# Optimization experiments

Measured on AMD Instinct MI355X. Metric: run time of the kernel, lower is better.

## Reference

```python
import jax, jax.numpy as jnp
import numpy as np

NEG_SLOPE = 0.01  # torch leaky_relu default

def _lrelu(x):
    return jax.nn.leaky_relu(x, NEG_SLOPE)

def _l2norm(x, axis):
    # torch F.normalize(p=2, eps=1e-12)
    n = jnp.linalg.norm(x, axis=axis, keepdims=True)
    return x / jnp.maximum(n, 1e-12)

def setup_inputs() -> dict:
    key = jax.random.key(0)
    ks = jax.random.split(key, 12)
    Nda, Nq, C, Din, Dout = 10000, 64, 1024, 128, 256
    target_adj = (jax.random.uniform(ks[0], (Nda, Nda)) < 0.002).astype(jnp.float32)
    query_adj = (jax.random.uniform(ks[1], (Nq, Nq)) < 0.2).astype(jnp.float32)
    node_features_da = jax.random.normal(ks[2], (Nda, Din), dtype=jnp.float32)
    node_features_q = jax.random.normal(ks[3], (Nq, Din), dtype=jnp.float32)
    candidate_set = jax.random.randint(ks[4], (C,), 0, Nda)
    candidate_adj = (jax.random.uniform(ks[5], (C, C)) < 0.01).astype(jnp.float32)
    s_in = 1.0 / np.sqrt(Din).astype(np.float32)
    s_out = 1.0 / np.sqrt(Dout).astype(np.float32)
    W1_da = jax.random.normal(ks[6], (Din, Dout), dtype=jnp.float32) * s_in
    W1_q = jax.random.normal(ks[7], (Din, Dout), dtype=jnp.float32) * s_in
    W2_da = jax.random.normal(ks[8], (Dout, Dout), dtype=jnp.float32) * s_out
    W2_q = jax.random.normal(ks[9], (Dout, Dout), dtype=jnp.float32) * s_out
    threshold = jnp.float32(0.2)
    return {"target_adj": target_adj, "node_features_da": node_features_da,
            "query_adj": query_adj, "node_features_q": node_features_q,
            "candidate_set": candidate_set, "candidate_adj": candidate_adj,
            "threshold": threshold, "W1_da": W1_da, "W1_q": W1_q,
            "W2_da": W2_da, "W2_q": W2_q}

def _cross_cosine(q, da, candidate_set):
    # cosine similarity between each query node and each candidate target node: [Nq, C]
    return _l2norm(q, 1) @ _l2norm(da[candidate_set], 1).T

def reference(target_adj, node_features_da, query_adj, node_features_q,
              candidate_set, candidate_adj, threshold, W1_da, W1_q, W2_da, W2_q):
    # layer 1: GCN propagation on both graphs (gcn(adj,x) = adj @ x @ W)
    da1 = _lrelu(target_adj @ (node_features_da @ W1_da))   # [Nda, D]
    q1 = _lrelu(query_adj @ (node_features_q @ W1_q))       # [Nq, D]
    c1 = _cross_cosine(q1, da1, candidate_set)               # [Nq, C]
    pre_da1 = da1[candidate_set]                             # [C, D]
    # NOTE: da1[candidate_set].data = ... mutates a temporary in torch -> no-op on da1
    att_da1 = _lrelu(da1)                                    # dropout in eval = identity
    h1_q = c1 @ pre_da1                                      # [Nq, D]
    att_q1 = _lrelu(q1 + _l2norm(h1_q, 0))
    # layer 2
    da2 = _lrelu(target_adj @ (att_da1 @ W2_da))
    q2 = _lrelu(query_adj @ (att_q1 @ W2_q))
    c2 = _cross_cosine(q2, da2, candidate_set)
    pre_da2 = da2[candidate_set]
    att_da2 = _lrelu(da2)                                    # in-place update is again a no-op
    h2_q = c2 @ pre_da2
    att_q2 = _lrelu(q2 + _l2norm(h2_q, 0))
    # graph-level matching score per target node
    emb = jnp.mean(att_q2, axis=0, keepdims=True)            # [1, D]
    num = att_da2 @ emb[0]                                   # [Nda]
    den = jnp.maximum(jnp.linalg.norm(att_da2, axis=1) * jnp.linalg.norm(emb), 1e-8)
    end = (num / den)[None, :]                               # [1, Nda]
    # threshold selection expressed with a mask (jit-safe, same math: excluded
    # rows/cols are zero and do not affect L2 norms, sums, or the trace)
    m = (end[0] > threshold).astype(att_da2.dtype)           # [Nda]
    F_ = att_da2 * m[:, None]
    re_adj = F_ @ F_.T                                       # [Nda, Nda]
    nor_re = _l2norm(re_adj, 1) * target_adj                 # elementwise with original adj
    cnt = jnp.sum(m)
    total = jnp.sum(nor_re)
    tr = jnp.trace(nor_re)
    has = cnt > 0
    pre_avg_degree = jnp.where(has, total / jnp.maximum(cnt, 1.0), 0.0)
    pre_avg_nodes = jnp.where(has, tr, 0.0)
    pre_density = jnp.where(has, 2.0 * total / (tr * (tr - 1.0) + 1e-4), 0.0)
    return (end, att_da2, att_q2, pre_avg_degree, pre_density, pre_avg_nodes)
```

## Files before the change

### kernel.cpp

```cpp
#include <hip/hip_runtime.h>

constexpr int NDA = 10000;
constexpr int NQ  = 64;
constexpr int CND = 1024;
constexpr int DIN = 128;
constexpr int D   = 256;
constexpr int CAP = 96;

#define LRELU(x) ((x) >= 0.f ? (x) : 0.01f * (x))

__device__ __forceinline__ float wave_red64(float v) {
#pragma unroll
    for (int o = 32; o; o >>= 1) v += __shfl_down(v, o);
    return v;
}

__global__ __launch_bounds__(256) void build_csr(const float* __restrict__ adj,
                                                 int* __restrict__ cols,
                                                 int* __restrict__ rowcnt) {
    int row = blockIdx.x;
    __shared__ int scnt;
    if (threadIdx.x == 0) scnt = 0;
    __syncthreads();
    const float4* rp = (const float4*)(adj + (size_t)row * NDA);
    for (int i = threadIdx.x; i < NDA / 4; i += 256) {
        float4 v = rp[i];
        if (v.x != 0.f) { int s = atomicAdd(&scnt, 1); if (s < CAP) cols[row * CAP + s] = 4 * i; }
        if (v.y != 0.f) { int s = atomicAdd(&scnt, 1); if (s < CAP) cols[row * CAP + s] = 4 * i + 1; }
        if (v.z != 0.f) { int s = atomicAdd(&scnt, 1); if (s < CAP) cols[row * CAP + s] = 4 * i + 2; }
        if (v.w != 0.f) { int s = atomicAdd(&scnt, 1); if (s < CAP) cols[row * CAP + s] = 4 * i + 3; }
    }
    __syncthreads();
    if (threadIdx.x == 0) rowcnt[row] = min(scnt, CAP);
}

template <int W, bool RELU_IN>
__global__ void spmm(const int* __restrict__ cols,
                     const int* __restrict__ rowcnt,
                     const float* __restrict__ X,
                     float* __restrict__ out) {
    int row = blockIdx.x;
    int d = threadIdx.x;
    int cnt = rowcnt[row];
    __shared__ int sc[CAP];
    if (d < CAP && d < cnt) sc[d] = cols[row * CAP + d];
    __syncthreads();
    float a0 = 0.f, a1 = 0.f, a2 = 0.f, a3 = 0.f;
    int k = 0;
    for (; k + 4 <= cnt; k += 4) {
        float v0 = X[(size_t)sc[k + 0] * W + d];
        float v1 = X[(size_t)sc[k + 1] * W + d];
        float v2 = X[(size_t)sc[k + 2] * W + d];
        float v3 = X[(size_t)sc[k + 3] * W + d];
        if (RELU_IN) { v0 = LRELU(v0); v1 = LRELU(v1); v2 = LRELU(v2); v3 = LRELU(v3); }
        a0 += v0; a1 += v1; a2 += v2; a3 += v3;
    }
    for (; k < cnt; k++) {
        float v = X[(size_t)sc[k] * W + d];
        if (RELU_IN) v = LRELU(v);
        a0 += v;
    }
    out[(size_t)row * W + d] = (a0 + a1) + (a2 + a3);
}

template <bool RELU_C, bool DUAL>
__global__ __launch_bounds__(256) void gemm64(const float* __restrict__ A,
                                              const float* __restrict__ B,
                                              float* __restrict__ C,
                                              float* __restrict__ C2,
                                              int M, int N, int K) {
    __shared__ float As[16][68];
    __shared__ float Bs[16][68];
    const int bm = blockIdx.x * 64;
    const int bn = blockIdx.y * 64;
    const int tid = threadIdx.x;
    const int tx = tid & 15, ty = tid >> 4;
    float acc[4][4] = {};
    for (int k0 = 0; k0 < K; k0 += 16) {
        {
            int m = tid >> 2;
            int k4 = (tid & 3) * 4;
            float4 v = make_float4(0.f, 0.f, 0.f, 0.f);
            if (bm + m < M) v = *(const float4*)(A + (size_t)(bm + m) * K + k0 + k4);
            As[k4 + 0][m] = v.x; As[k4 + 1][m] = v.y; As[k4 + 2][m] = v.z; As[k4 + 3][m] = v.w;
        }
        {
            int kk = tid >> 4;
            int n4 = (tid & 15) * 4;
            float4 v = *(const float4*)(B + (size_t)(k0 + kk) * N + bn + n4);
            Bs[kk][n4 + 0] = v.x; Bs[kk][n4 + 1] = v.y; Bs[kk][n4 + 2] = v.z; Bs[kk][n4 + 3] = v.w;
        }
        __syncthreads();
#pragma unroll
        for (int kk = 0; kk < 16; kk++) {
            float av[4], bv[4];
#pragma unroll
            for (int i = 0; i < 4; i++) av[i] = As[kk][ty * 4 + i];
#pragma unroll
            for (int j = 0; j < 4; j++) bv[j] = Bs[kk][tx * 4 + j];
#pragma unroll
            for (int i = 0; i < 4; i++)
#pragma unroll
                for (int j = 0; j < 4; j++) acc[i][j] += av[i] * bv[j];
        }
        __syncthreads();
    }
#pragma unroll
    for (int i = 0; i < 4; i++) {
        int r = bm + ty * 4 + i;
        if (r < M) {
            float4 v;
            v.x = acc[i][0]; v.y = acc[i][1]; v.z = acc[i][2]; v.w = acc[i][3];
            if (RELU_C) { v.x = LRELU(v.x); v.y = LRELU(v.y); v.z = LRELU(v.z); v.w = LRELU(v.w); }
            *(float4*)(C + (size_t)r * N + bn + tx * 4) = v;
            if (DUAL) {
                float4 u;
                u.x = LRELU(v.x); u.y = LRELU(v.y); u.z = LRELU(v.z); u.w = LRELU(v.w);
                *(float4*)(C2 + (size_t)r * N + bn + tx * 4) = u;
            }
        }
    }
}

__global__ __launch_bounds__(256) void qpath_kernel(const float* __restrict__ Fq,
                                                    const float* __restrict__ Wq,
                                                    const float* __restrict__ Qadj,
                                                    float* __restrict__ q_out,
                                                    int K) {
    __shared__ float As[16][68];
    __shared__ float Bs[16][68];
    __shared__ float Xs[64][68];
    __shared__ float Qs[64][68];
    const int bn = blockIdx.x * 64;
    const int tid = threadIdx.x;
    const int tx = tid & 15, ty = tid >> 4;
    float acc[4][4] = {};
    for (int k0 = 0; k0 < K; k0 += 16) {
        {
            int m = tid >> 2;
            int k4 = (tid & 3) * 4;
            float4 v = *(const float4*)(Fq + (size_t)m * K + k0 + k4);
            As[k4 + 0][m] = v.x; As[k4 + 1][m] = v.y; As[k4 + 2][m] = v.z; As[k4 + 3][m] = v.w;
        }
        {
            int kk = tid >> 4;
            int n4 = (tid & 15) * 4;
            float4 v = *(const float4*)(Wq + (size_t)(k0 + kk) * D + bn + n4);
            Bs[kk][n4 + 0] = v.x; Bs[kk][n4 + 1] = v.y; Bs[kk][n4 + 2] = v.z; Bs[kk][n4 + 3] = v.w;
        }
        __syncthreads();
#pragma unroll
        for (int kk = 0; kk < 16; kk++) {
            float av[4], bv[4];
#pragma unroll
            for (int i = 0; i < 4; i++) av[i] = As[kk][ty * 4 + i];
#pragma unroll
            for (int j = 0; j < 4; j++) bv[j] = Bs[kk][tx * 4 + j];
#pragma unroll
            for (int i = 0; i < 4; i++)
#pragma unroll
                for (int j = 0; j < 4; j++) acc[i][j] += av[i] * bv[j];
        }
        __syncthreads();
    }
#pragma unroll
    for (int i = 0; i < 4; i++)
#pragma unroll
        for (int j = 0; j < 4; j++) Xs[ty * 4 + i][tx * 4 + j] = acc[i][j];
    for (int l = tid; l < NQ * NQ; l += 256) Qs[l >> 6][l & 63] = Qadj[l];
    __syncthreads();
    float a2[4][4] = {};
#pragma unroll 4
    for (int kk = 0; kk < NQ; kk++) {
        float av[4], bv[4];
#pragma unroll
        for (int i = 0; i < 4; i++) av[i] = Qs[ty * 4 + i][kk];
#pragma unroll
        for (int j = 0; j < 4; j++) bv[j] = Xs[kk][tx * 4 + j];
#pragma unroll
        for (int i = 0; i < 4; i++)
#pragma unroll
            for (int j = 0; j < 4; j++) a2[i][j] += av[i] * bv[j];
    }
#pragma unroll
    for (int i = 0; i < 4; i++)
#pragma unroll
        for (int j = 0; j < 4; j++)
            q_out[(ty * 4 + i) * D + bn + tx * 4 + j] = LRELU(a2[i][j]);
}

__global__ __launch_bounds__(256) void rownorms_kernel(const float* __restrict__ da,
                                                       const int* __restrict__ cand,
                                                       float* __restrict__ rncinv,
                                                       const float* __restrict__ q,
                                                       float* __restrict__ rnqinv) {
    int b = blockIdx.x;
    const float* src;
    float* dst;
    if (b < CND) { src = da + (size_t)cand[b] * D; dst = rncinv + b; }
    else         { src = q + (size_t)(b - CND) * D; dst = rnqinv + (b - CND); }
    float v = src[threadIdx.x];
    float p = wave_red64(v * v);
    __shared__ float red[4];
    int w = threadIdx.x >> 6, lane = threadIdx.x & 63;
    if (lane == 0) red[w] = p;
    __syncthreads();
    if (threadIdx.x == 0) *dst = 1.f / fmaxf(sqrtf(red[0] + red[1] + red[2] + red[3]), 1e-12f);
}

__global__ __launch_bounds__(256) void candM_kernel(const float* __restrict__ da,
                                                    const int* __restrict__ cand,
                                                    const float* __restrict__ rncinv,
                                                    float* __restrict__ M) {
    __shared__ float SA[8][64], SB[8][64];
    const int ti = blockIdx.x, tj = blockIdx.y;
    const int tid = threadIdx.x;
    const int tx = tid & 15, ty = tid >> 4;
    float acc[4][4] = {};
    for (int c0 = 0; c0 < CND; c0 += 8) {
        for (int l = tid; l < 512; l += 256) {
            int rr = l >> 6, c = l & 63;
            int cr = cand[c0 + rr];
            float s = rncinv[c0 + rr];
            SA[rr][c] = da[(size_t)cr * D + ti * 64 + c] * s;
            SB[rr][c] = da[(size_t)cr * D + tj * 64 + c];
        }
        __syncthreads();
#pragma unroll
        for (int rr = 0; rr < 8; rr++) {
            float av[4], bv[4];
#pragma unroll
            for (int i = 0; i < 4; i++) av[i] = SA[rr][ty * 4 + i];
#pragma unroll
            for (int j = 0; j < 4; j++) bv[j] = SB[rr][tx * 4 + j];
#pragma unroll
            for (int i = 0; i < 4; i++)
#pragma unroll
                for (int j = 0; j < 4; j++) acc[i][j] += av[i] * bv[j];
        }
        __syncthreads();
    }
#pragma unroll
    for (int i = 0; i < 4; i++)
#pragma unroll
        for (int j = 0; j < 4; j++)
            M[(ti * 64 + ty * 4 + i) * D + tj * 64 + tx * 4 + j] = acc[i][j];
}

__global__ __launch_bounds__(256) void hq_gemm(const float* __restrict__ q,
                                               const float* __restrict__ rnqinv,
                                               const float* __restrict__ M,
                                               float* __restrict__ h) {
    __shared__ float As[16][68];
    __shared__ float Bs[16][68];
    const int bn = blockIdx.x * 64;
    const int tid = threadIdx.x;
    const int tx = tid & 15, ty = tid >> 4;
    float acc[4][4] = {};
    for (int k0 = 0; k0 < D; k0 += 16) {
        {
            int m = tid >> 2;
            int k4 = (tid & 3) * 4;
            float s = rnqinv[m];
            float4 v = *(const float4*)(q + (size_t)m * D + k0 + k4);
            As[k4 + 0][m] = v.x * s; As[k4 + 1][m] = v.y * s;
            As[k4 + 2][m] = v.z * s; As[k4 + 3][m] = v.w * s;
        }
        {
            int kk = tid >> 4;
            int n4 = (tid & 15) * 4;
            float4 v = *(const float4*)(M + (size_t)(k0 + kk) * D + bn + n4);
            Bs[kk][n4 + 0] = v.x; Bs[kk][n4 + 1] = v.y; Bs[kk][n4 + 2] = v.z; Bs[kk][n4 + 3] = v.w;
        }
        __syncthreads();
#pragma unroll
        for (int kk = 0; kk < 16; kk++) {
            float av[4], bv[4];
#pragma unroll
            for (int i = 0; i < 4; i++) av[i] = As[kk][ty * 4 + i];
#pragma unroll
            for (int j = 0; j < 4; j++) bv[j] = Bs[kk][tx * 4 + j];
#pragma unroll
            for (int i = 0; i < 4; i++)
#pragma unroll
                for (int j = 0; j < 4; j++) acc[i][j] += av[i] * bv[j];
        }
        __syncthreads();
    }
#pragma unroll
    for (int i = 0; i < 4; i++)
#pragma unroll
        for (int j = 0; j < 4; j++)
            h[(ty * 4 + i) * D + bn + tx * 4 + j] = acc[i][j];
}

__global__ __launch_bounds__(256) void attq_kernel(const float* __restrict__ q,
                                                   const float* __restrict__ h,
                                                   float* __restrict__ attq,
                                                   float* __restrict__ emb) {
    int d = threadIdx.x;
    float hv[NQ];
    float ss = 0.f;
#pragma unroll
    for (int r = 0; r < NQ; r++) {
        hv[r] = h[r * D + d];
        ss += hv[r] * hv[r];
    }
    float inv = 1.f / fmaxf(sqrtf(ss), 1e-12f);
    float es = 0.f;
#pragma unroll
    for (int r = 0; r < NQ; r++) {
        float v = q[r * D + d] + hv[r] * inv;
        v = LRELU(v);
        attq[r * D + d] = v;
        es += v;
    }
    if (emb) {
        float e = es * (1.f / (float)NQ);
        emb[d] = e;
        float p = wave_red64(e * e);
        __shared__ float red[4];
        int w = d >> 6, lane = d & 63;
        if (lane == 0) red[w] = p;
        __syncthreads();
        if (d == 0) emb[D] = sqrtf(red[0] + red[1] + red[2] + red[3]);
    }
}

__global__ __launch_bounds__(256) void end_kernel(const float* __restrict__ A,
                                                  const float* __restrict__ emb,
                                                  const float* __restrict__ thr_p,
                                                  float* __restrict__ endv,
                                                  float* __restrict__ m,
                                                  float* __restrict__ cnt) {
    __shared__ float se[D];
    __shared__ float scnt;
    int d = threadIdx.x;
    se[d] = emb[d];
    if (d == 0) scnt = 0.f;
    __syncthreads();
    float embn = emb[D];
    float thr = *thr_p;
    int w = d >> 6, lane = d & 63;
    int row = blockIdx.x * 4 + w;
    const float* ar = A + (size_t)row * D;
    float num = 0.f, sq = 0.f;
#pragma unroll
    for (int s = 0; s < 4; s++) {
        float v = ar[lane + 64 * s];
        num += v * se[lane + 64 * s];
        sq += v * v;
    }
#pragma unroll
    for (int o = 32; o; o >>= 1) { num += __shfl_down(num, o); sq += __shfl_down(sq, o); }
    if (lane == 0) {
        float den = fmaxf(sqrtf(sq) * embn, 1e-8f);
        float e = num / den;
        endv[row] = e;
        float mv = e > thr ? 1.f : 0.f;
        m[row] = mv;
        if (mv != 0.f) atomicAdd(&scnt, 1.f);
    }
    __syncthreads();
    if (d == 0 && scnt != 0.f) atomicAdd(cnt, scnt);
}

constexpr int GCHUNK = 400;
__global__ __launch_bounds__(256) void G_kernel(const float* __restrict__ A,
                                                const float* __restrict__ m,
                                                float* __restrict__ G) {
    __shared__ float SA[8][64], SB[8][64];
    int ti = blockIdx.x >> 2, tj = blockIdx.x & 3;
    int base = blockIdx.y * GCHUNK;
    int tid = threadIdx.x;
    int tx = tid & 15, ty = tid >> 4;
    float acc[4][4] = {};
    for (int g0 = 0; g0 < GCHUNK; g0 += 8) {
        for (int l = tid; l < 512; l += 256) {
            int rr = l >> 6, c = l & 63;
            int r = base + g0 + rr;
            float mv = m[r];
            SA[rr][c] = A[(size_t)r * D + ti * 64 + c] * mv;
            SB[rr][c] = A[(size_t)r * D + tj * 64 + c];
        }
        __syncthreads();
#pragma unroll
        for (int rr = 0; rr < 8; rr++) {
            float av[4], bv[4];
#pragma unroll
            for (int i = 0; i < 4; i++) av[i] = SA[rr][ty * 4 + i];
#pragma unroll
            for (int j = 0; j < 4; j++) bv[j] = SB[rr][tx * 4 + j];
#pragma unroll
            for (int i = 0; i < 4; i++)
#pragma unroll
                for (int j = 0; j < 4; j++) acc[i][j] += av[i] * bv[j];
        }
        __syncthreads();
    }
#pragma unroll
    for (int i = 0; i < 4; i++)
#pragma unroll
        for (int j = 0; j < 4; j++)
            atomicAdd(&G[(ti * 64 + ty * 4 + i) * D + tj * 64 + tx * 4 + j], acc[i][j]);
}

__global__ __launch_bounds__(256) void final_kernel(const int* __restrict__ cols,
                                                    const int* __restrict__ rowcnt,
                                                    const float* __restrict__ m,
                                                    const float* __restrict__ A,
                                                    const float* __restrict__ H,
                                                    double* __restrict__ total,
                                                    double* __restrict__ tr) {
    int i = blockIdx.x;
    if (m[i] == 0.f) return;
    __shared__ float sa[D];
    __shared__ int sc[CAP];
    __shared__ float red[4], red2[4];
    __shared__ float sdenom;
    int d = threadIdx.x;
    float av = A[(size_t)i * D + d];
    sa[d] = av;
    int cnt = rowcnt[i];
    if (d < cnt) sc[d] = cols[i * CAP + d];
    float p = wave_red64(av * H[(size_t)i * D + d]);
    int w = d >> 6, lane = d & 63;
    if (lane == 0) red[w] = p;
    __syncthreads();
    if (d == 0) sdenom = fmaxf(sqrtf(red[0] + red[1] + red[2] + red[3]), 1e-12f);
    __syncthreads();
    float accs = 0.f, acct = 0.f;
    for (int k = w; k < cnt; k += 4) {
        int j = sc[k];
        if (m[j] != 0.f) {
            const float* aj = A + (size_t)j * D;
            float t = sa[lane] * aj[lane] + sa[lane + 64] * aj[lane + 64]
                    + sa[lane + 128] * aj[lane + 128] + sa[lane + 192] * aj[lane + 192];
            t = wave_red64(t);
            if (lane == 0) { accs += t; if (j == i) acct += t; }
        }
    }
    if (lane == 0) { red[w] = accs; red2[w] = acct; }
    __syncthreads();
    if (d == 0) {
        float s = red[0] + red[1] + red[2] + red[3];
        float t2 = red2[0] + red2[1] + red2[2] + red2[3];
        double inv = 1.0 / (double)sdenom;
        if (s != 0.f) atomicAdd(total, (double)s * inv);
        if (t2 != 0.f) atomicAdd(tr, (double)t2 * inv);
    }
}

__global__ void scalars_kernel(const float* __restrict__ cnt,
                               const double* __restrict__ total,
                               const double* __restrict__ tr,
                               float* __restrict__ out) {
    float c = *cnt;
    float T = (float)*total;
    float R = (float)*tr;
    bool has = c > 0.f;
    out[0] = has ? (T / fmaxf(c, 1.f)) : 0.f;
    out[1] = has ? (2.f * T / (R * (R - 1.f) + 1e-4f)) : 0.f;
    out[2] = has ? R : 0.f;
}

extern "C" void kernel_launch(void* const* d_in, const int* in_sizes, int n_in,
                              void* d_out, int out_size, void* d_ws, size_t ws_size,
                              hipStream_t stream) {
    (void)in_sizes; (void)n_in; (void)out_size; (void)ws_size;
    const float* adj  = (const float*)d_in[0];
    const float* Fda  = (const float*)d_in[1];
    const float* Qadj = (const float*)d_in[2];
    const float* Fq   = (const float*)d_in[3];
    const int*   cand = (const int*)d_in[4];
    const float* thr  = (const float*)d_in[6];
    const float* W1da = (const float*)d_in[7];
    const float* W1q  = (const float*)d_in[8];
    const float* W2da = (const float*)d_in[9];
    const float* W2q  = (const float*)d_in[10];

    float* out = (float*)d_out;
    float* o_end    = out;
    float* o_attda2 = out + NDA;
    float* o_attq2  = out + NDA + (size_t)NDA * D;
    float* o_sc     = o_attq2 + NQ * D;

    char* w = (char*)d_ws;
    size_t off = 0;
    auto alloc = [&](size_t b) { size_t r = off; off += (b + 255) & ~(size_t)255; return r; };
    float* bufA = (float*)(w + alloc((size_t)NDA * D * 4));
    float* bufB = (float*)(w + alloc((size_t)NDA * D * 4));
    float* bufC = (float*)(w + alloc((size_t)NDA * D * 4));
    int* colsb   = (int*)(w + alloc((size_t)NDA * CAP * 4));
    int* rowcntb = (int*)(w + alloc((size_t)NDA * 4));
    float* mbuf  = (float*)(w + alloc((size_t)NDA * 4));
    char* zbase = w + alloc(262144 + 256);
    float* Gb    = (float*)zbase;
    float* cntb  = (float*)(zbase + 262144);
    double* totb = (double*)(zbase + 262144 + 8);
    double* trb  = (double*)(zbase + 262144 + 16);
    float* q1b  = (float*)(w + alloc((size_t)NQ * D * 4));
    float* aq1  = (float*)(w + alloc((size_t)NQ * D * 4));
    float* q2b  = (float*)(w + alloc((size_t)NQ * D * 4));
    float* hb   = (float*)(w + alloc((size_t)NQ * D * 4));
    float* Mb   = (float*)(w + alloc((size_t)D * D * 4));
    float* rncinv = (float*)(w + alloc((size_t)CND * 4));
    float* rnqinv = (float*)(w + alloc((size_t)NQ * 4));
    float* embb   = (float*)(w + alloc((size_t)(D + 1) * 4));

    hipMemsetAsync(zbase, 0, 262144 + 256, stream);

    const dim3 gBig((NDA + 63) / 64, D / 64);

    build_csr<<<NDA, 256, 0, stream>>>(adj, colsb, rowcntb);
    qpath_kernel<<<D / 64, 256, 0, stream>>>(Fq, W1q, Qadj, q1b, DIN);
    spmm<DIN, false><<<NDA, DIN, 0, stream>>>(colsb, rowcntb, Fda, bufA);
    gemm64<true, false><<<gBig, 256, 0, stream>>>(bufA, W1da, bufB, nullptr, NDA, D, DIN);
    rownorms_kernel<<<CND + NQ, 256, 0, stream>>>(bufB, cand, rncinv, q1b, rnqinv);
    candM_kernel<<<dim3(4, 4), 256, 0, stream>>>(bufB, cand, rncinv, Mb);
    hq_gemm<<<D / 64, 256, 0, stream>>>(q1b, rnqinv, Mb, hb);
    attq_kernel<<<1, 256, 0, stream>>>(q1b, hb, aq1, nullptr);
    qpath_kernel<<<D / 64, 256, 0, stream>>>(aq1, W2q, Qadj, q2b, D);
    spmm<D, true><<<NDA, D, 0, stream>>>(colsb, rowcntb, bufB, bufA);
    gemm64<true, true><<<gBig, 256, 0, stream>>>(bufA, W2da, bufC, o_attda2, NDA, D, D);
    rownorms_kernel<<<CND + NQ, 256, 0, stream>>>(bufC, cand, rncinv, q2b, rnqinv);
    candM_kernel<<<dim3(4, 4), 256, 0, stream>>>(bufC, cand, rncinv, Mb);
    hq_gemm<<<D / 64, 256, 0, stream>>>(q2b, rnqinv, Mb, hb);
    attq_kernel<<<1, 256, 0, stream>>>(q2b, hb, o_attq2, embb);
    end_kernel<<<NDA / 4, 256, 0, stream>>>(o_attda2, embb, thr, o_end, mbuf, cntb);
    G_kernel<<<dim3(16, NDA / GCHUNK), 256, 0, stream>>>(o_attda2, mbuf, Gb);
    gemm64<false, false><<<gBig, 256, 0, stream>>>(o_attda2, Gb, bufB, nullptr, NDA, D, D);
    final_kernel<<<NDA, 256, 0, stream>>>(colsb, rowcntb, mbuf, o_attda2, bufB, totb, trb);
    scalars_kernel<<<1, 1, 0, stream>>>(cntb, totb, trb, o_sc);
}
```

Baseline: 1.252 ms.

## Split candidate Gram GEMM over K with atomics and fuse query norms

The candidate Gram matrix kernel, which ran only 16 blocks, is now split along the candidate dimension into 8 chunks that accumulate into M with atomicAdd. M is zeroed by hq_gemm after it reads it, so the buffer is ready for the next layer. Query row sum-of-squares are accumulated inside qpath_kernel and turned into inverse norms in hq_gemm, which removes the query half of the rownorms kernel. G_kernel's chunk size also grows, giving fewer blocks and fewer atomics. The float atomics make the summation order nondeterministic and add extra global atomic traffic.

```diff
diff --git a/kernel.cpp b/kernel.cpp
--- a/kernel.cpp
+++ b/kernel.cpp
@@ -126,11 +126,13 @@
                                                     const float* __restrict__ Wq,
                                                     const float* __restrict__ Qadj,
                                                     float* __restrict__ q_out,
+                                                    float* __restrict__ rnqsq,
                                                     int K) {
     __shared__ float As[16][68];
     __shared__ float Bs[16][68];
     __shared__ float Xs[64][68];
     __shared__ float Qs[64][68];
+    __shared__ float sq[64];
     const int bn = blockIdx.x * 64;
     const int tid = threadIdx.x;
     const int tx = tid & 15, ty = tid >> 4;
@@ -168,6 +170,7 @@
 #pragma unroll
         for (int j = 0; j < 4; j++) Xs[ty * 4 + i][tx * 4 + j] = acc[i][j];
     for (int l = tid; l < NQ * NQ; l += 256) Qs[l >> 6][l & 63] = Qadj[l];
+    if (tid < 64) sq[tid] = 0.f;
     __syncthreads();
     float a2[4][4] = {};
 #pragma unroll 4
@@ -183,45 +186,51 @@
             for (int j = 0; j < 4; j++) a2[i][j] += av[i] * bv[j];
     }
 #pragma unroll
-    for (int i = 0; i < 4; i++)
-#pragma unroll
-        for (int j = 0; j < 4; j++)
-            q_out[(ty * 4 + i) * D + bn + tx * 4 + j] = LRELU(a2[i][j]);
-}
-
-__global__ __launch_bounds__(256) void rownorms_kernel(const float* __restrict__ da,
-                                                       const int* __restrict__ cand,
-                                                       float* __restrict__ rncinv,
-                                                       const float* __restrict__ q,
-                                                       float* __restrict__ rnqinv) {
+    for (int i = 0; i < 4; i++) {
+        float rp = 0.f;
+#pragma unroll
+        for (int j = 0; j < 4; j++) {
+            float v = LRELU(a2[i][j]);
+            q_out[(ty * 4 + i) * D + bn + tx * 4 + j] = v;
+            rp += v * v;
+        }
+        atomicAdd(&sq[ty * 4 + i], rp);
+    }
+    __syncthreads();
+    if (tid < 64) atomicAdd(&rnqsq[tid], sq[tid]);
+}
+
+__global__ __launch_bounds__(256) void candnorms_kernel(const float* __restrict__ da,
+                                                        const int* __restrict__ cand,
+                                                        float* __restrict__ rncinv) {
     int b = blockIdx.x;
-    const float* src;
-    float* dst;
-    if (b < CND) { src = da + (size_t)cand[b] * D; dst = rncinv + b; }
-    else         { src = q + (size_t)(b - CND) * D; dst = rnqinv + (b - CND); }
+    const float* src = da + (size_t)cand[b] * D;
     float v = src[threadIdx.x];
     float p = wave_red64(v * v);
     __shared__ float red[4];
     int w = threadIdx.x >> 6, lane = threadIdx.x & 63;
     if (lane == 0) red[w] = p;
     __syncthreads();
-    if (threadIdx.x == 0) *dst = 1.f / fmaxf(sqrtf(red[0] + red[1] + red[2] + red[3]), 1e-12f);
-}
-
-__global__ __launch_bounds__(256) void candM_kernel(const float* __restrict__ da,
-                                                    const int* __restrict__ cand,
-                                                    const float* __restrict__ rncinv,
-                                                    float* __restrict__ M) {
+    if (threadIdx.x == 0)
+        rncinv[b] = 1.f / fmaxf(sqrtf(red[0] + red[1] + red[2] + red[3]), 1e-12f);
+}
+
+constexpr int CCH = 128;
+__global__ __launch_bounds__(256) void candM_split(const float* __restrict__ da,
+                                                   const int* __restrict__ cand,
+                                                   const float* __restrict__ rncinv,
+                                                   float* __restrict__ M) {
     __shared__ float SA[8][64], SB[8][64];
     const int ti = blockIdx.x, tj = blockIdx.y;
+    const int cb = blockIdx.z * CCH;
     const int tid = threadIdx.x;
     const int tx = tid & 15, ty = tid >> 4;
     float acc[4][4] = {};
-    for (int c0 = 0; c0 < CND; c0 += 8) {
+    for (int c0 = 0; c0 < CCH; c0 += 8) {
         for (int l = tid; l < 512; l += 256) {
             int rr = l >> 6, c = l & 63;
-            int cr = cand[c0 + rr];
-            float s = rncinv[c0 + rr];
+            int cr = cand[cb + c0 + rr];
+            float s = rncinv[cb + c0 + rr];
             SA[rr][c] = da[(size_t)cr * D + ti * 64 + c] * s;
             SB[rr][c] = da[(size_t)cr * D + tj * 64 + c];
         }
@@ -244,12 +253,12 @@
     for (int i = 0; i < 4; i++)
 #pragma unroll
         for (int j = 0; j < 4; j++)
-            M[(ti * 64 + ty * 4 + i) * D + tj * 64 + tx * 4 + j] = acc[i][j];
+            atomicAdd(&M[(ti * 64 + ty * 4 + i) * D + tj * 64 + tx * 4 + j], acc[i][j]);
 }
 
 __global__ __launch_bounds__(256) void hq_gemm(const float* __restrict__ q,
-                                               const float* __restrict__ rnqinv,
-                                               const float* __restrict__ M,
+                                               const float* __restrict__ rnqsq,
+                                               float* __restrict__ M,
                                                float* __restrict__ h) {
     __shared__ float As[16][68];
     __shared__ float Bs[16][68];
@@ -257,11 +266,12 @@
     const int tid = threadIdx.x;
     const int tx = tid & 15, ty = tid >> 4;
     float acc[4][4] = {};
+    const float4 z4 = make_float4(0.f, 0.f, 0.f, 0.f);
     for (int k0 = 0; k0 < D; k0 += 16) {
         {
             int m = tid >> 2;
             int k4 = (tid & 3) * 4;
-            float s = rnqinv[m];
+            float s = 1.f / fmaxf(sqrtf(rnqsq[m]), 1e-12f);
             float4 v = *(const float4*)(q + (size_t)m * D + k0 + k4);
             As[k4 + 0][m] = v.x * s; As[k4 + 1][m] = v.y * s;
             As[k4 + 2][m] = v.z * s; As[k4 + 3][m] = v.w * s;
@@ -270,6 +280,7 @@
             int kk = tid >> 4;
             int n4 = (tid & 15) * 4;
             float4 v = *(const float4*)(M + (size_t)(k0 + kk) * D + bn + n4);
+            *(float4*)(M + (size_t)(k0 + kk) * D + bn + n4) = z4;
             Bs[kk][n4 + 0] = v.x; Bs[kk][n4 + 1] = v.y; Bs[kk][n4 + 2] = v.z; Bs[kk][n4 + 3] = v.w;
         }
         __syncthreads();
@@ -297,8 +308,10 @@
 __global__ __launch_bounds__(256) void attq_kernel(const float* __restrict__ q,
                                                    const float* __restrict__ h,
                                                    float* __restrict__ attq,
-                                                   float* __restrict__ emb) {
+                                                   float* __restrict__ emb,
+                                                   float* __restrict__ rnqsq) {
     int d = threadIdx.x;
+    if (d < 64) rnqsq[d] = 0.f;
     float hv[NQ];
     float ss = 0.f;
 #pragma unroll
@@ -365,7 +378,7 @@
     if (d == 0 && scnt != 0.f) atomicAdd(cnt, scnt);
 }
 
-constexpr int GCHUNK = 400;
+constexpr int GCHUNK = 1000;
 __global__ __launch_bounds__(256) void G_kernel(const float* __restrict__ A,
                                                 const float* __restrict__ m,
                                                 float* __restrict__ G) {
@@ -494,39 +507,39 @@
     int* colsb   = (int*)(w + alloc((size_t)NDA * CAP * 4));
     int* rowcntb = (int*)(w + alloc((size_t)NDA * 4));
     float* mbuf  = (float*)(w + alloc((size_t)NDA * 4));
-    char* zbase = w + alloc(262144 + 256);
-    float* Gb    = (float*)zbase;
-    float* cntb  = (float*)(zbase + 262144);
-    double* totb = (double*)(zbase + 262144 + 8);
-    double* trb  = (double*)(zbase + 262144 + 16);
+    char* zbase = w + alloc(525000);
+    float* Gb     = (float*)zbase;
+    float* Mb     = (float*)(zbase + 262144);
+    float* rnqsqb = (float*)(zbase + 524288);
+    float* cntb   = (float*)(zbase + 524544);
+    double* totb  = (double*)(zbase + 524552);
+    double* trb   = (double*)(zbase + 524560);
     float* q1b  = (float*)(w + alloc((size_t)NQ * D * 4));
     float* aq1  = (float*)(w + alloc((size_t)NQ * D * 4));
     float* q2b  = (float*)(w + alloc((size_t)NQ * D * 4));
     float* hb   = (float*)(w + alloc((size_t)NQ * D * 4));
-    float* Mb   = (float*)(w + alloc((size_t)D * D * 4));
     float* rncinv = (float*)(w + alloc((size_t)CND * 4));
-    float* rnqinv = (float*)(w + alloc((size_t)NQ * 4));
     float* embb   = (float*)(w + alloc((size_t)(D + 1) * 4));
 
-    hipMemsetAsync(zbase, 0, 262144 + 256, stream);
+    hipMemsetAsync(zbase, 0, 524576, stream);
 
     const dim3 gBig((NDA + 63) / 64, D / 64);
 
     build_csr<<<NDA, 256, 0, stream>>>(adj, colsb, rowcntb);
-    qpath_kernel<<<D / 64, 256, 0, stream>>>(Fq, W1q, Qadj, q1b, DIN);
+    qpath_kernel<<<D / 64, 256, 0, stream>>>(Fq, W1q, Qadj, q1b, rnqsqb, DIN);
     spmm<DIN, false><<<NDA, DIN, 0, stream>>>(colsb, rowcntb, Fda, bufA);
     gemm64<true, false><<<gBig, 256, 0, stream>>>(bufA, W1da, bufB, nullptr, NDA, D, DIN);
-    rownorms_kernel<<<CND + NQ, 256, 0, stream>>>(bufB, cand, rncinv, q1b, rnqinv);
-    candM_kernel<<<dim3(4, 4), 256, 0, stream>>>(bufB, cand, rncinv, Mb);
-    hq_gemm<<<D / 64, 256, 0, stream>>>(q1b, rnqinv, Mb, hb);
-    attq_kernel<<<1, 256, 0, stream>>>(q1b, hb, aq1, nullptr);
-    qpath_kernel<<<D / 64, 256, 0, stream>>>(aq1, W2q, Qadj, q2b, D);
+    candnorms_kernel<<<CND, 256, 0, stream>>>(bufB, cand, rncinv);
+    candM_split<<<dim3(4, 4, CND / CCH), 256, 0, stream>>>(bufB, cand, rncinv, Mb);
+    hq_gemm<<<D / 64, 256, 0, stream>>>(q1b, rnqsqb, Mb, hb);
+    attq_kernel<<<1, 256, 0, stream>>>(q1b, hb, aq1, nullptr, rnqsqb);
+    qpath_kernel<<<D / 64, 256, 0, stream>>>(aq1, W2q, Qadj, q2b, rnqsqb, D);
     spmm<D, true><<<NDA, D, 0, stream>>>(colsb, rowcntb, bufB, bufA);
     gemm64<true, true><<<gBig, 256, 0, stream>>>(bufA, W2da, bufC, o_attda2, NDA, D, D);
-    rownorms_kernel<<<CND + NQ, 256, 0, stream>>>(bufC, cand, rncinv, q2b, rnqinv);
-    candM_kernel<<<dim3(4, 4), 256, 0, stream>>>(bufC, cand, rncinv, Mb);
-    hq_gemm<<<D / 64, 256, 0, stream>>>(q2b, rnqinv, Mb, hb);
-    attq_kernel<<<1, 256, 0, stream>>>(q2b, hb, o_attq2, embb);
+    candnorms_kernel<<<CND, 256, 0, stream>>>(bufC, cand, rncinv);
+    candM_split<<<dim3(4, 4, CND / CCH), 256, 0, stream>>>(bufC, cand, rncinv, Mb);
+    hq_gemm<<<D / 64, 256, 0, stream>>>(q2b, rnqsqb, Mb, hb);
+    attq_kernel<<<1, 256, 0, stream>>>(q2b, hb, o_attq2, embb, rnqsqb);
     end_kernel<<<NDA / 4, 256, 0, stream>>>(o_attda2, embb, thr, o_end, mbuf, cntb);
     G_kernel<<<dim3(16, NDA / GCHUNK), 256, 0, stream>>>(o_attda2, mbuf, Gb);
     gemm64<false, false><<<gBig, 256, 0, stream>>>(o_attda2, Gb, bufB, nullptr, NDA, D, D);
```

Measured after the change: 1.080 ms. 1.16x faster.
